# Performance work log

Measured on AMD Instinct MI355X. Metric: run time of the kernel, lower is better.

The kernel has to match this reference:

```python
import jax, jax.numpy as jnp
import numpy as np

NUM_LAGS_P1 = 4
N_NODES = 2048


def setup_inputs() -> dict:
    key = jax.random.key(0)
    # Scale so that ||A*A||_1 ~ O(1): entries ~ N(0, s^2), A_sq entries ~ s^2,
    # row sums of A_sq ~ n*s^2. s = 0.02 -> n*s^2 ~ 0.82 for n=2048.
    scale = 0.02
    adjacencies = scale * jax.random.normal(
        key, (NUM_LAGS_P1, N_NODES, N_NODES), dtype=jnp.float32
    )
    return {"adjacencies": adjacencies}


def reference(adjacencies) -> jnp.ndarray:
    # Only the contemporaneous slice A_0 needs the acyclicity constraint.
    A = adjacencies[0]                     # [n, n]
    n = A.shape[0]
    A_sq = A * A                           # elementwise square (NOTEARS h(A))
    E = jax.scipy.linalg.expm(A_sq)        # Pade + scaling-and-squaring
    h = jnp.trace(E) - n                   # scalar constraint value
    return h
```

## Files before the change

### kernel.cpp

```cpp
#include <hip/hip_runtime.h>
#include <hip/hip_bf16.h>

#define NN 2048
typedef unsigned short us;
typedef __attribute__((ext_vector_type(8))) short short8;
typedef __attribute__((ext_vector_type(4))) float f4;
typedef __attribute__((ext_vector_type(4))) float f32x4;
typedef __attribute__((ext_vector_type(8))) unsigned short us8;

__device__ __forceinline__ us f2bf(float f) {
    unsigned int u = __float_as_uint(f);
    u += 0x7fffu + ((u >> 16) & 1u);
    return (us)(u >> 16);
}
__device__ __forceinline__ float bf2f(us h) {
    return __uint_as_float(((unsigned int)h) << 16);
}
__device__ __forceinline__ void gload16(const us* g, us* l) {
    __builtin_amdgcn_global_load_lds(
        (const __attribute__((address_space(1))) unsigned int*)g,
        (__attribute__((address_space(3))) unsigned int*)l, 16, 0, 0);
}

__global__ void prep_kernel(const float* __restrict__ A0,
                            us* __restrict__ Bbf, us* __restrict__ BbfT,
                            float* __restrict__ rs, float* __restrict__ cs,
                            double* __restrict__ pt1, double* __restrict__ accs) {
    __shared__ float sq[64][65];
    const int I = blockIdx.y, J = blockIdx.x;
    const int tid = threadIdx.x, lane = tid & 63, wv = tid >> 6;
    const size_t rI = (size_t)I * 64, rJ = (size_t)J * 64;

    #pragma unroll
    for (int u = tid; u < 512; u += 256) {
        const int row = u >> 3, c8 = (u & 7) * 8;
        f4 a0 = *(const f4*)&A0[(rI + row) * NN + rJ + c8];
        f4 a1 = *(const f4*)&A0[(rI + row) * NN + rJ + c8 + 4];
        us8 o;
        #pragma unroll
        for (int k = 0; k < 4; ++k) { float s = a0[k] * a0[k]; sq[row][c8 + k] = s; o[k] = f2bf(s); }
        #pragma unroll
        for (int k = 0; k < 4; ++k) { float s = a1[k] * a1[k]; sq[row][c8 + 4 + k] = s; o[4 + k] = f2bf(s); }
        *(us8*)&Bbf[(rI + row) * NN + rJ + c8] = o;
    }
    __syncthreads();

    #pragma unroll
    for (int u = tid; u < 512; u += 256) {
        const int r = u >> 3, c0 = (u & 7) * 8;
        us8 o;
        #pragma unroll
        for (int k = 0; k < 8; ++k) o[k] = f2bf(sq[c0 + k][r]);
        *(us8*)&BbfT[(rJ + r) * NN + rI + c0] = o;
    }

    if (I == J) {
        if (tid < 64) { rs[rI + tid] = 0.f; cs[rI + tid] = 0.f; }
        if (I == 0 && tid == 64) accs[0] = 0.0;
        if (wv == 0) {
            double t1 = sq[lane][lane];
            #pragma unroll
            for (int s = 32; s > 0; s >>= 1) t1 += __shfl_down(t1, s, 64);
            if (lane == 0) pt1[I] = t1;
        }
    }
}

__launch_bounds__(256, 4)
__global__ void gemm_kernel(const us* __restrict__ A, const us* __restrict__ BT,
                            us* __restrict__ c2, float* __restrict__ rs,
                            float* __restrict__ cs, double* __restrict__ accs) {
    __shared__ us lA[4096];
    __shared__ us lB[4096];
    const int tid  = threadIdx.x;
    const int lane = tid & 63;
    const int w    = tid >> 6;
    const int wr   = w >> 1, wc = w & 1;
    const int rowBase = blockIdx.y * 128;
    const int colBase = blockIdx.x * 128;
    const int kbase   = blockIdx.z * 512;
    us* __restrict__ C = c2 + (size_t)blockIdx.z * (NN * (size_t)NN);
    const int lr = lane & 15;
    const int lk = (lane >> 4) * 8;

    const int srow = tid >> 2;
    const int scol = (tid & 3) * 8;
    const us* gA0 = A  + (size_t)(rowBase + srow) * NN + kbase + scol;
    const us* gA1 = A  + (size_t)(rowBase + 64 + srow) * NN + kbase + scol;
    const us* gB0 = BT + (size_t)(colBase + srow) * NN + kbase + scol;
    const us* gB1 = BT + (size_t)(colBase + 64 + srow) * NN + kbase + scol;
    const int d0 = srow * 32 + scol;
    const int d1 = (64 + srow) * 32 + scol;

    f32x4 acc[4][4] = {};

    for (int t = 0; t < 16; ++t) {
        const int k = t * 32;
        gload16(gA0 + k, &lA[d0]);
        gload16(gA1 + k, &lA[d1]);
        gload16(gB0 + k, &lB[d0]);
        gload16(gB1 + k, &lB[d1]);
        __syncthreads();

        short8 af[4], bfr[4];
        #pragma unroll
        for (int mi = 0; mi < 4; ++mi)
            af[mi] = *(const short8*)&lA[(wr * 64 + mi * 16 + lr) * 32 + lk];
        #pragma unroll
        for (int ni = 0; ni < 4; ++ni)
            bfr[ni] = *(const short8*)&lB[(wc * 64 + ni * 16 + lr) * 32 + lk];
        #pragma unroll
        for (int mi = 0; mi < 4; ++mi)
            #pragma unroll
            for (int ni = 0; ni < 4; ++ni)
                acc[mi][ni] = __builtin_amdgcn_mfma_f32_16x16x32_bf16(
                    af[mi], bfr[ni], acc[mi][ni], 0, 0, 0);
        __syncthreads();
    }

    const int orow = (lane >> 4) * 4;
    const int ocol = lane & 15;
    const bool diagblk = (rowBase == colBase);
    double tdiag = 0.0;
    float colp[4] = {0.f, 0.f, 0.f, 0.f};
    #pragma unroll
    for (int mi = 0; mi < 4; ++mi) {
        #pragma unroll
        for (int r = 0; r < 4; ++r) {
            const int gr = rowBase + wr * 64 + mi * 16 + orow + r;
            float rowp = 0.f;
            #pragma unroll
            for (int ni = 0; ni < 4; ++ni) {
                float v = acc[mi][ni][r];
                const int gc = colBase + wc * 64 + ni * 16 + ocol;
                C[(size_t)gr * NN + gc] = f2bf(v);
                rowp += v;
                colp[ni] += v;
                if (diagblk && gr == gc) tdiag += (double)v;
            }
            rowp += __shfl_xor(rowp, 1, 64);
            rowp += __shfl_xor(rowp, 2, 64);
            rowp += __shfl_xor(rowp, 4, 64);
            rowp += __shfl_xor(rowp, 8, 64);
            if ((lane & 15) == 0) atomicAdd(&rs[gr], rowp);
        }
    }
    #pragma unroll
    for (int ni = 0; ni < 4; ++ni) {
        colp[ni] += __shfl_xor(colp[ni], 16, 64);
        colp[ni] += __shfl_xor(colp[ni], 32, 64);
        if (lane < 16) atomicAdd(&cs[colBase + wc * 64 + ni * 16 + ocol], colp[ni]);
    }
    if (diagblk) {
        #pragma unroll
        for (int s = 32; s > 0; s >>= 1) tdiag += __shfl_down(tdiag, s, 64);
        if (lane == 0 && tdiag != 0.0) atomicAdd(&accs[0], tdiag);
    }
}

__global__ void corr_kernel(const us* __restrict__ c2,
                            const us* __restrict__ BbfT,
                            double* __restrict__ pt3, double* __restrict__ pt4) {
    __shared__ float cT[64][65];
    __shared__ double wred[2][4];
    const size_t PS = (size_t)NN * NN;
    const int I = blockIdx.y, J = blockIdx.x;
    const int tid = threadIdx.x, lane = tid & 63, wv = tid >> 6;
    const size_t rI = (size_t)I * 64, rJ = (size_t)J * 64;

    double t3 = 0;
    float myC[2][8];
    #pragma unroll
    for (int ph = 0; ph < 2; ++ph) {
        const int u = tid + ph * 256;
        const int row = u >> 3, c8 = (u & 7) * 8;
        const size_t off  = (rI + row) * NN + rJ + c8;
        const size_t off2 = (rJ + row) * NN + rI + c8;
        us8 v0 = *(const us8*)&c2[off];
        us8 v1 = *(const us8*)&c2[off + PS];
        us8 v2 = *(const us8*)&c2[off + 2 * PS];
        us8 v3 = *(const us8*)&c2[off + 3 * PS];
        us8 vt = *(const us8*)&BbfT[off];
        us8 w0 = *(const us8*)&c2[off2];
        us8 w1 = *(const us8*)&c2[off2 + PS];
        us8 w2 = *(const us8*)&c2[off2 + 2 * PS];
        us8 w3 = *(const us8*)&c2[off2 + 3 * PS];
        #pragma unroll
        for (int k = 0; k < 8; ++k) {
            float c = (bf2f(v0[k]) + bf2f(v1[k])) + (bf2f(v2[k]) + bf2f(v3[k]));
            myC[ph][k] = c;
            t3 += (double)(c * bf2f(vt[k]));
            cT[row][c8 + k] = (bf2f(w0[k]) + bf2f(w1[k])) + (bf2f(w2[k]) + bf2f(w3[k]));
        }
    }
    __syncthreads();

    double t4 = 0;
    #pragma unroll
    for (int ph = 0; ph < 2; ++ph) {
        const int u = tid + ph * 256;
        const int row = u >> 3, c8 = (u & 7) * 8;
        #pragma unroll
        for (int k = 0; k < 8; ++k)
            t4 += (double)(myC[ph][k] * cT[c8 + k][row]);
    }

    #pragma unroll
    for (int s = 32; s > 0; s >>= 1) {
        t3 += __shfl_down(t3, s, 64);
        t4 += __shfl_down(t4, s, 64);
    }
    if (lane == 0) { wred[0][wv] = t3; wred[1][wv] = t4; }
    __syncthreads();
    if (tid == 0) {
        const int b = blockIdx.y * 32 + blockIdx.x;
        pt3[b] = wred[0][0] + wred[0][1] + wred[0][2] + wred[0][3];
        pt4[b] = wred[1][0] + wred[1][1] + wred[1][2] + wred[1][3];
    }
}

__global__ void finalize_kernel(const float* __restrict__ rs,
                                const float* __restrict__ cs,
                                const double* __restrict__ pt1,
                                const double* __restrict__ accs,
                                const double* __restrict__ pt3,
                                const double* __restrict__ pt4,
                                float* __restrict__ out) {
    __shared__ double red[256];
    const int t = threadIdx.x;
    double t1 = 0, t3 = 0, t4 = 0, s2 = 0, s4 = 0;
    if (t < 32) t1 = pt1[t];
    for (int i = t; i < 1024; i += 256) { t3 += pt3[i]; t4 += pt4[i]; }
    for (int i = t; i < NN; i += 256) {
        double r = rs[i];
        s2 += r; s4 += r * (double)cs[i];
    }
    double vals[5] = {t1, t3, t4, s2, s4};
    double tot[5];
    for (int v = 0; v < 5; ++v) {
        red[t] = vals[v]; __syncthreads();
        for (int s = 128; s > 0; s >>= 1) { if (t < s) red[t] += red[t + s]; __syncthreads(); }
        tot[v] = red[0]; __syncthreads();
    }
    if (t == 0) {
        double t2 = accs[0];
        double lam2 = tot[4] / tot[3];
        double lam  = sqrt(lam2);
        double tail = exp(lam) - 1.0 - lam - lam2 * 0.5
                      - lam * lam2 * (1.0 / 6.0) - lam2 * lam2 * (1.0 / 24.0);
        out[0] = (float)(tot[0] + t2 * 0.5 + tot[1] * (1.0 / 6.0)
                         + tot[2] * (1.0 / 24.0) + tail);
    }
}

extern "C" void kernel_launch(void* const* d_in, const int* in_sizes, int n_in,
                              void* d_out, int out_size, void* d_ws, size_t ws_size,
                              hipStream_t stream) {
    const float* A0 = (const float*)d_in[0];
    char* ws = (char*)d_ws;
    us*     Bbf  = (us*)(ws);
    us*     BbfT = (us*)(ws + 8388608);
    us*     c2   = (us*)(ws + 16777216);
    float*  rs   = (float*)(ws + 50331648);
    float*  cs   = (float*)(ws + 50339840);
    double* pt1  = (double*)(ws + 50348032);
    double* accs = (double*)(ws + 50348544);
    double* pt3  = (double*)(ws + 50349056);
    double* pt4  = (double*)(ws + 50357248);
    float*  out  = (float*)d_out;

    prep_kernel<<<dim3(32, 32), 256, 0, stream>>>(A0, Bbf, BbfT, rs, cs, pt1, accs);
    gemm_kernel<<<dim3(16, 16, 4), 256, 0, stream>>>(Bbf, BbfT, c2, rs, cs, accs);
    corr_kernel<<<dim3(32, 32), 256, 0, stream>>>(c2, BbfT, pt3, pt4);
    finalize_kernel<<<1, 256, 0, stream>>>(rs, cs, pt1, accs, pt3, pt4, out);
}
```

Baseline: 148.9 us.

## Double-buffer GEMM LDS tiles, store transposed product, move row/col sums to corr

The GEMM main loop now uses two LDS buffers and issues the global-to-LDS loads for the next k-tile before computing on the current one, so load latency can overlap the MFMA work. The epilogue writes the partial product transposed as 4-element vector stores and drops its per-element row and column shuffles and atomics. Row and column sums are instead computed in the correction kernel from the summed split-K tiles, which then reads Bbf instead of BbfT. In exchange, LDS use doubles, which may limit occupancy, and the correction kernel takes on extra reductions and atomics.

```diff
diff --git a/kernel.cpp b/kernel.cpp
--- a/kernel.cpp
+++ b/kernel.cpp
@@ -7,6 +7,7 @@
 typedef __attribute__((ext_vector_type(4))) float f4;
 typedef __attribute__((ext_vector_type(4))) float f32x4;
 typedef __attribute__((ext_vector_type(8))) unsigned short us8;
+typedef __attribute__((ext_vector_type(4))) unsigned short us4;
 
 __device__ __forceinline__ us f2bf(float f) {
     unsigned int u = __float_as_uint(f);
@@ -24,7 +25,7 @@
 
 __global__ void prep_kernel(const float* __restrict__ A0,
                             us* __restrict__ Bbf, us* __restrict__ BbfT,
-                            float* __restrict__ rs, float* __restrict__ cs,
+                            float* __restrict__ rsD, float* __restrict__ csD,
                             double* __restrict__ pt1, double* __restrict__ accs) {
     __shared__ float sq[64][65];
     const int I = blockIdx.y, J = blockIdx.x;
@@ -55,7 +56,7 @@
     }
 
     if (I == J) {
-        if (tid < 64) { rs[rI + tid] = 0.f; cs[rI + tid] = 0.f; }
+        if (tid < 64) { rsD[rI + tid] = 0.f; csD[rI + tid] = 0.f; }
         if (I == 0 && tid == 64) accs[0] = 0.0;
         if (wv == 0) {
             double t1 = sq[lane][lane];
@@ -68,10 +69,9 @@
 
 __launch_bounds__(256, 4)
 __global__ void gemm_kernel(const us* __restrict__ A, const us* __restrict__ BT,
-                            us* __restrict__ c2, float* __restrict__ rs,
-                            float* __restrict__ cs, double* __restrict__ accs) {
-    __shared__ us lA[4096];
-    __shared__ us lB[4096];
+                            us* __restrict__ D, double* __restrict__ accs) {
+    __shared__ us lA[2][4096];
+    __shared__ us lB[2][4096];
     const int tid  = threadIdx.x;
     const int lane = tid & 63;
     const int w    = tid >> 6;
@@ -79,7 +79,7 @@
     const int rowBase = blockIdx.y * 128;
     const int colBase = blockIdx.x * 128;
     const int kbase   = blockIdx.z * 512;
-    us* __restrict__ C = c2 + (size_t)blockIdx.z * (NN * (size_t)NN);
+    us* __restrict__ Dp = D + (size_t)blockIdx.z * ((size_t)NN * NN);
     const int lr = lane & 15;
     const int lk = (lane >> 4) * 8;
 
@@ -94,21 +94,28 @@
 
     f32x4 acc[4][4] = {};
 
+    gload16(gA0, &lA[0][d0]);
+    gload16(gA1, &lA[0][d1]);
+    gload16(gB0, &lB[0][d0]);
+    gload16(gB1, &lB[0][d1]);
+    __syncthreads();
+
     for (int t = 0; t < 16; ++t) {
-        const int k = t * 32;
-        gload16(gA0 + k, &lA[d0]);
-        gload16(gA1 + k, &lA[d1]);
-        gload16(gB0 + k, &lB[d0]);
-        gload16(gB1 + k, &lB[d1]);
-        __syncthreads();
-
+        const int cur = t & 1;
+        if (t < 15) {
+            const int k = (t + 1) * 32;
+            gload16(gA0 + k, &lA[cur ^ 1][d0]);
+            gload16(gA1 + k, &lA[cur ^ 1][d1]);
+            gload16(gB0 + k, &lB[cur ^ 1][d0]);
+            gload16(gB1 + k, &lB[cur ^ 1][d1]);
+        }
         short8 af[4], bfr[4];
         #pragma unroll
         for (int mi = 0; mi < 4; ++mi)
-            af[mi] = *(const short8*)&lA[(wr * 64 + mi * 16 + lr) * 32 + lk];
+            af[mi] = *(const short8*)&lA[cur][(wr * 64 + mi * 16 + lr) * 32 + lk];
         #pragma unroll
         for (int ni = 0; ni < 4; ++ni)
-            bfr[ni] = *(const short8*)&lB[(wc * 64 + ni * 16 + lr) * 32 + lk];
+            bfr[ni] = *(const short8*)&lB[cur][(wc * 64 + ni * 16 + lr) * 32 + lk];
         #pragma unroll
         for (int mi = 0; mi < 4; ++mi)
             #pragma unroll
@@ -122,46 +129,33 @@
     const int ocol = lane & 15;
     const bool diagblk = (rowBase == colBase);
     double tdiag = 0.0;
-    float colp[4] = {0.f, 0.f, 0.f, 0.f};
-    #pragma unroll
-    for (int mi = 0; mi < 4; ++mi) {
-        #pragma unroll
-        for (int r = 0; r < 4; ++r) {
-            const int gr = rowBase + wr * 64 + mi * 16 + orow + r;
-            float rowp = 0.f;
+    #pragma unroll
+    for (int mi = 0; mi < 4; ++mi)
+        #pragma unroll
+        for (int ni = 0; ni < 4; ++ni) {
+            const int gr0 = rowBase + wr * 64 + mi * 16 + orow;
+            const int gc  = colBase + wc * 64 + ni * 16 + ocol;
+            us4 o;
             #pragma unroll
-            for (int ni = 0; ni < 4; ++ni) {
-                float v = acc[mi][ni][r];
-                const int gc = colBase + wc * 64 + ni * 16 + ocol;
-                C[(size_t)gr * NN + gc] = f2bf(v);
-                rowp += v;
-                colp[ni] += v;
-                if (diagblk && gr == gc) tdiag += (double)v;
+            for (int r = 0; r < 4; ++r) o[r] = f2bf(acc[mi][ni][r]);
+            *(us4*)&Dp[(size_t)gc * NN + gr0] = o;
+            if (diagblk) {
+                #pragma unroll
+                for (int r = 0; r < 4; ++r)
+                    if (gc == gr0 + r) tdiag += (double)acc[mi][ni][r];
             }
-            rowp += __shfl_xor(rowp, 1, 64);
-            rowp += __shfl_xor(rowp, 2, 64);
-            rowp += __shfl_xor(rowp, 4, 64);
-            rowp += __shfl_xor(rowp, 8, 64);
-            if ((lane & 15) == 0) atomicAdd(&rs[gr], rowp);
-        }
-    }
-    #pragma unroll
-    for (int ni = 0; ni < 4; ++ni) {
-        colp[ni] += __shfl_xor(colp[ni], 16, 64);
-        colp[ni] += __shfl_xor(colp[ni], 32, 64);
-        if (lane < 16) atomicAdd(&cs[colBase + wc * 64 + ni * 16 + ocol], colp[ni]);
-    }
+        }
     if (diagblk) {
         #pragma unroll
         for (int s = 32; s > 0; s >>= 1) tdiag += __shfl_down(tdiag, s, 64);
-        if (lane == 0 && tdiag != 0.0) atomicAdd(&accs[0], tdiag);
-    }
-}
-
-__global__ void corr_kernel(const us* __restrict__ c2,
-                            const us* __restrict__ BbfT,
+        if (lane == 0) atomicAdd(&accs[0], tdiag);
+    }
+}
+
+__global__ void corr_kernel(const us* __restrict__ D, const us* __restrict__ Bbf,
+                            float* __restrict__ rsD, float* __restrict__ csD,
                             double* __restrict__ pt3, double* __restrict__ pt4) {
-    __shared__ float cT[64][65];
+    __shared__ float dT[64][65];
     __shared__ double wred[2][4];
     const size_t PS = (size_t)NN * NN;
     const int I = blockIdx.y, J = blockIdx.x;
@@ -169,40 +163,62 @@
     const size_t rI = (size_t)I * 64, rJ = (size_t)J * 64;
 
     double t3 = 0;
-    float myC[2][8];
+    float myD[2][8];
+    float rowp[2];
     #pragma unroll
     for (int ph = 0; ph < 2; ++ph) {
         const int u = tid + ph * 256;
         const int row = u >> 3, c8 = (u & 7) * 8;
         const size_t off  = (rI + row) * NN + rJ + c8;
         const size_t off2 = (rJ + row) * NN + rI + c8;
-        us8 v0 = *(const us8*)&c2[off];
-        us8 v1 = *(const us8*)&c2[off + PS];
-        us8 v2 = *(const us8*)&c2[off + 2 * PS];
-        us8 v3 = *(const us8*)&c2[off + 3 * PS];
-        us8 vt = *(const us8*)&BbfT[off];
-        us8 w0 = *(const us8*)&c2[off2];
-        us8 w1 = *(const us8*)&c2[off2 + PS];
-        us8 w2 = *(const us8*)&c2[off2 + 2 * PS];
-        us8 w3 = *(const us8*)&c2[off2 + 3 * PS];
+        us8 v0 = *(const us8*)&D[off];
+        us8 v1 = *(const us8*)&D[off + PS];
+        us8 v2 = *(const us8*)&D[off + 2 * PS];
+        us8 v3 = *(const us8*)&D[off + 3 * PS];
+        us8 vb = *(const us8*)&Bbf[off];
+        us8 w0 = *(const us8*)&D[off2];
+        us8 w1 = *(const us8*)&D[off2 + PS];
+        us8 w2 = *(const us8*)&D[off2 + 2 * PS];
+        us8 w3 = *(const us8*)&D[off2 + 3 * PS];
+        float rp = 0.f;
         #pragma unroll
         for (int k = 0; k < 8; ++k) {
-            float c = (bf2f(v0[k]) + bf2f(v1[k])) + (bf2f(v2[k]) + bf2f(v3[k]));
-            myC[ph][k] = c;
-            t3 += (double)(c * bf2f(vt[k]));
-            cT[row][c8 + k] = (bf2f(w0[k]) + bf2f(w1[k])) + (bf2f(w2[k]) + bf2f(w3[k]));
-        }
+            float d = (bf2f(v0[k]) + bf2f(v1[k])) + (bf2f(v2[k]) + bf2f(v3[k]));
+            myD[ph][k] = d;
+            rp += d;
+            t3 += (double)(d * bf2f(vb[k]));
+            dT[row][c8 + k] = (bf2f(w0[k]) + bf2f(w1[k])) + (bf2f(w2[k]) + bf2f(w3[k]));
+        }
+        rowp[ph] = rp;
     }
     __syncthreads();
 
     double t4 = 0;
+    float colp[2];
     #pragma unroll
     for (int ph = 0; ph < 2; ++ph) {
         const int u = tid + ph * 256;
         const int row = u >> 3, c8 = (u & 7) * 8;
-        #pragma unroll
-        for (int k = 0; k < 8; ++k)
-            t4 += (double)(myC[ph][k] * cT[c8 + k][row]);
+        float cp = 0.f;
+        #pragma unroll
+        for (int k = 0; k < 8; ++k) {
+            float x = dT[c8 + k][row];
+            t4 += (double)(myD[ph][k] * x);
+            cp += x;
+        }
+        colp[ph] = cp;
+    }
+
+    #pragma unroll
+    for (int ph = 0; ph < 2; ++ph) {
+        float rp = rowp[ph], cp = colp[ph];
+        rp += __shfl_xor(rp, 1, 64); rp += __shfl_xor(rp, 2, 64); rp += __shfl_xor(rp, 4, 64);
+        cp += __shfl_xor(cp, 1, 64); cp += __shfl_xor(cp, 2, 64); cp += __shfl_xor(cp, 4, 64);
+        const int row = (tid + ph * 256) >> 3;
+        if ((tid & 7) == 0) {
+            atomicAdd(&rsD[rI + row], rp);
+            atomicAdd(&csD[rI + row], cp);
+        }
     }
 
     #pragma unroll
@@ -219,8 +235,8 @@
     }
 }
 
-__global__ void finalize_kernel(const float* __restrict__ rs,
-                                const float* __restrict__ cs,
+__global__ void finalize_kernel(const float* __restrict__ rsD,
+                                const float* __restrict__ csD,
                                 const double* __restrict__ pt1,
                                 const double* __restrict__ accs,
                                 const double* __restrict__ pt3,
@@ -232,8 +248,8 @@
     if (t < 32) t1 = pt1[t];
     for (int i = t; i < 1024; i += 256) { t3 += pt3[i]; t4 += pt4[i]; }
     for (int i = t; i < NN; i += 256) {
-        double r = rs[i];
-        s2 += r; s4 += r * (double)cs[i];
+        double r = rsD[i];
+        s2 += r; s4 += r * (double)csD[i];
     }
     double vals[5] = {t1, t3, t4, s2, s4};
     double tot[5];
@@ -260,17 +276,17 @@
     char* ws = (char*)d_ws;
     us*     Bbf  = (us*)(ws);
     us*     BbfT = (us*)(ws + 8388608);
-    us*     c2   = (us*)(ws + 16777216);
-    float*  rs   = (float*)(ws + 50331648);
-    float*  cs   = (float*)(ws + 50339840);
+    us*     Dmat = (us*)(ws + 16777216);
+    float*  rsD  = (float*)(ws + 50331648);
+    float*  csD  = (float*)(ws + 50339840);
     double* pt1  = (double*)(ws + 50348032);
     double* accs = (double*)(ws + 50348544);
     double* pt3  = (double*)(ws + 50349056);
     double* pt4  = (double*)(ws + 50357248);
     float*  out  = (float*)d_out;
 
-    prep_kernel<<<dim3(32, 32), 256, 0, stream>>>(A0, Bbf, BbfT, rs, cs, pt1, accs);
-    gemm_kernel<<<dim3(16, 16, 4), 256, 0, stream>>>(Bbf, BbfT, c2, rs, cs, accs);
-    corr_kernel<<<dim3(32, 32), 256, 0, stream>>>(c2, BbfT, pt3, pt4);
-    finalize_kernel<<<1, 256, 0, stream>>>(rs, cs, pt1, accs, pt3, pt4, out);
-}
+    prep_kernel<<<dim3(32, 32), 256, 0, stream>>>(A0, Bbf, BbfT, rsD, csD, pt1, accs);
+    gemm_kernel<<<dim3(16, 16, 4), 256, 0, stream>>>(Bbf, BbfT, Dmat, accs);
+    corr_kernel<<<dim3(32, 32), 256, 0, stream>>>(Dmat, Bbf, rsD, csD, pt3, pt4);
+    finalize_kernel<<<1, 256, 0, stream>>>(rsD, csD, pt1, accs, pt3, pt4, out);
+}
```

Result: faster. 139.4 us (-6.4%).
